# Optimization experiments

Hardware: AMD Instinct MI355X
Metric: run time of the kernel (lower is better)

## Reference

```python
import jax, jax.numpy as jnp
import numpy as np

B, S, E, H = 4, 2048, 1024, 16
D = E // H  # head_dim = 64

def setup_inputs() -> dict:
    key = jax.random.key(0)
    ks = jax.random.split(key, 9)
    std = 1.0 / np.sqrt(E)
    return {
        "x":  jax.random.normal(ks[0], (B, S, E), jnp.float32),
        "Wq": jax.random.uniform(ks[1], (E, E), jnp.float32, -std, std),
        "bq": jax.random.uniform(ks[2], (E,),   jnp.float32, -std, std),
        "Wk": jax.random.uniform(ks[3], (E, E), jnp.float32, -std, std),
        "bk": jax.random.uniform(ks[4], (E,),   jnp.float32, -std, std),
        "Wv": jax.random.uniform(ks[5], (E, E), jnp.float32, -std, std),
        "bv": jax.random.uniform(ks[6], (E,),   jnp.float32, -std, std),
        "Wo": jax.random.uniform(ks[7], (E, E), jnp.float32, -std, std),
        "bo": jax.random.uniform(ks[8], (E,),   jnp.float32, -std, std),
    }

def reference(x, Wq, bq, Wk, bk, Wv, bv, Wo, bo):
    b, s, e = x.shape
    # QKV projections (weights stored as [in,out] == torch W.T applied as x @ W)
    q = (x @ Wq + bq).reshape(b, s, H, D).transpose(0, 2, 1, 3)  # [B,H,S,D]
    k = (x @ Wk + bk).reshape(b, s, H, D).transpose(0, 2, 1, 3)
    v = (x @ Wv + bv).reshape(b, s, H, D).transpose(0, 2, 1, 3)
    scores = jnp.einsum('bhqd,bhkd->bhqk', q, k) / jnp.sqrt(jnp.float32(D))
    causal = jnp.triu(jnp.ones((s, s), bool), k=1)  # True above diagonal
    scores = jnp.where(causal, -jnp.inf, scores)
    p = jax.nn.softmax(scores, axis=-1)  # dropout disabled (eval mode)
    out = jnp.einsum('bhqk,bhkd->bhqd', p, v)  # [B,H,S,D]
    out = out.transpose(0, 2, 1, 3).reshape(b, s, e)
    return out @ Wo + bo
```

## Files before the change

kernel.cpp:

```cpp
#include <hip/hip_runtime.h>
#include <math.h>

#define E_DIM 1024
#define B_DIM 4
#define S_DIM 2048
#define H_DIM 16
#define D_HEAD 64
#define M_DIM (B_DIM * S_DIM)
#define LOG2E 1.44269504f

typedef _Float16 half8 __attribute__((ext_vector_type(8)));
typedef _Float16 half4 __attribute__((ext_vector_type(4)));
typedef __fp16  fp16x2 __attribute__((ext_vector_type(2)));
typedef float floatx4 __attribute__((ext_vector_type(4)));
typedef unsigned uint2v __attribute__((ext_vector_type(2)));
#define MFMA_F16(a, b, c) __builtin_amdgcn_mfma_f32_16x16x32_f16(a, b, c, 0, 0, 0)

#if __has_builtin(__builtin_amdgcn_exp2f)
#define EXP2F(x) __builtin_amdgcn_exp2f(x)
#else
#define EXP2F(x) exp2f(x)
#endif

union H4 { fp16x2 h2[2]; half4 h4; };
union H8 { fp16x2 h2[4]; half8 h8; };

#define GLDS16(g, l)                                                          \
    __builtin_amdgcn_global_load_lds(                                         \
        (const __attribute__((address_space(1))) void*)(g),                   \
        (__attribute__((address_space(3))) void*)(l), 16, 0, 0)

__device__ const int SEG_QBLK[40] = {3,4,5,6,7,7,8,8,9,9,10,10,11,11,11,12,12,12,
                                     13,13,13,14,14,14,15,15,15,15,
                                     2,6,10,14, 1,5,9,13, 0,4,8,12};
__device__ const int SEG_SEG[40]  = {0,0,0,0,0,1,0,1,0,1,0,1,0,1,2,0,1,2,
                                     0,1,2,0,1,2,0,1,2,3,
                                     0,1,2,3, 0,1,2,3, 0,1,2,3};
__device__ const int SEG_BASE[16] = {0,1,2,3,4,6,8,10,12,15,18,21,24,28,32,36};

__global__ __launch_bounds__(256) void cvt_x(
    const float* __restrict__ X, _Float16* __restrict__ Xh)
{
    size_t i = ((size_t)blockIdx.x * 256 + threadIdx.x) * 8;
    float4 a = *(const float4*)&X[i];
    float4 b = *(const float4*)&X[i + 4];
    half8 h = {(_Float16)a.x, (_Float16)a.y, (_Float16)a.z, (_Float16)a.w,
               (_Float16)b.x, (_Float16)b.y, (_Float16)b.z, (_Float16)b.w};
    *(half8*)&Xh[i] = h;
}

__global__ __launch_bounds__(256) void cvt_w(
    const float* __restrict__ W0, const float* __restrict__ W1,
    const float* __restrict__ W2, const float* __restrict__ W3,
    _Float16* __restrict__ T0, _Float16* __restrict__ T1,
    _Float16* __restrict__ T2, _Float16* __restrict__ T3)
{
    const int z = blockIdx.z;
    const float* W = (z == 0) ? W0 : (z == 1) ? W1 : (z == 2) ? W2 : W3;
    _Float16*   T  = (z == 0) ? T0 : (z == 1) ? T1 : (z == 2) ? T2 : T3;
    const int k0 = blockIdx.x * 64, n0 = blockIdx.y * 64;
    const int tid = threadIdx.x;
    __shared__ float t[64][65];
#pragma unroll
    for (int it = 0; it < 4; it++) {
        int r = it * 16 + (tid >> 4);
        int c = (tid & 15) * 4;
        float4 v = *(const float4*)&W[(size_t)(k0 + r) * E_DIM + n0 + c];
        t[r][c] = v.x; t[r][c + 1] = v.y; t[r][c + 2] = v.z; t[r][c + 3] = v.w;
    }
    __syncthreads();
#pragma unroll
    for (int it = 0; it < 2; it++) {
        int n = it * 32 + (tid >> 3);
        int kk = (tid & 7) * 8;
        half8 h;
#pragma unroll
        for (int j = 0; j < 8; j++) h[j] = (_Float16)t[kk + j][n];
        *(half8*)&T[(size_t)(n0 + n) * E_DIM + k0 + kk] = h;
    }
}

#define GEMM_CORE(Aptr, Bptr)                                                 \
    const int tid = threadIdx.x;                                              \
    const int wave = tid >> 6, lane = tid & 63;                               \
    const int m16 = lane & 15, quad = lane >> 4;                              \
    const int wm = (wave >> 1) * 64, wn = (wave & 1) * 64;                    \
    const int m0 = blockIdx.x * 128, n0 = blockIdx.y * 128;                   \
    __shared__ _Float16 As[128 * 32];                                         \
    __shared__ _Float16 Bs[128 * 32];                                         \
    floatx4 acc[4][4];                                                        \
    const floatx4 zf = {0.f, 0.f, 0.f, 0.f};                                  \
    _Pragma("unroll") for (int i = 0; i < 4; i++)                             \
        _Pragma("unroll") for (int j = 0; j < 4; j++) acc[i][j] = zf;         \
    const int lrow = lane >> 2, lseg = lane & 3;                              \
    const _Float16* gA = (Aptr) + (size_t)(m0 + wave * 32 + lrow) * E_DIM + lseg * 8; \
    const _Float16* gB = (Bptr) + (size_t)(n0 + wave * 32 + lrow) * E_DIM + lseg * 8; \
    _Float16* lA = As + (wave * 32) * 32;                                     \
    _Float16* lB = Bs + (wave * 32) * 32;                                     \
    for (int k0 = 0; k0 < E_DIM; k0 += 32) {                                  \
        __syncthreads();                                                      \
        GLDS16(gA + k0, lA);                                                  \
        GLDS16(gA + 16 * E_DIM + k0, lA + 16 * 32);                           \
        GLDS16(gB + k0, lB);                                                  \
        GLDS16(gB + 16 * E_DIM + k0, lB + 16 * 32);                           \
        __syncthreads();                                                      \
        half8 af[4], bf[4];                                                   \
        _Pragma("unroll") for (int mt = 0; mt < 4; mt++)                      \
            af[mt] = *(const half8*)&As[(wm + mt * 16 + m16) * 32 + quad * 8];\
        _Pragma("unroll") for (int nt = 0; nt < 4; nt++)                      \
            bf[nt] = *(const half8*)&Bs[(wn + nt * 16 + m16) * 32 + quad * 8];\
        _Pragma("unroll") for (int mt = 0; mt < 4; mt++)                      \
            _Pragma("unroll") for (int nt = 0; nt < 4; nt++)                  \
                acc[mt][nt] = MFMA_F16(af[mt], bf[nt], acc[mt][nt]);          \
    }

#define STAGE256(t, s)                                                        \
    _Pragma("unroll") for (int i = 0; i < 4; i++) {                           \
        GLDS16(aS[i] + (t) * 64, As + (s) * 16384 + dOff[i]);                 \
        GLDS16(bS[i] + (t) * 64, Bs + (s) * 16384 + dOff[i]);                 \
    }

#define PH_READ_A(mh)                                                         \
    _Pragma("unroll") for (int am = 0; am < 4; am++)                          \
        _Pragma("unroll") for (int kh = 0; kh < 2; kh++)                      \
            a_[am][kh] = *(const half8*)&As[sb +                              \
                (wr * 128 + (mh) * 64 + am * 16 + m16) * 64 +                 \
                (((kh * 4 + quad) ^ sw8) * 8)];

#define PH_READ_B(nh)                                                         \
    _Pragma("unroll") for (int bn = 0; bn < 2; bn++)                          \
        _Pragma("unroll") for (int kh = 0; kh < 2; kh++)                      \
            b_[bn][kh] = *(const half8*)&Bs[sb +                              \
                (wc * 64 + (nh) * 32 + bn * 16 + m16) * 64 +                  \
                (((kh * 4 + quad) ^ sw8) * 8)];

#define PH_MFMA(mh, nh)                                                       \
    __builtin_amdgcn_s_setprio(1);                                            \
    _Pragma("unroll") for (int am = 0; am < 4; am++)                          \
        _Pragma("unroll") for (int bn = 0; bn < 2; bn++)                      \
            acc[(mh) * 4 + am][(nh) * 2 + bn] =                               \
                MFMA_F16(a_[am][1], b_[bn][1],                                \
                    MFMA_F16(a_[am][0], b_[bn][0],                            \
                             acc[(mh) * 4 + am][(nh) * 2 + bn]));             \
    __builtin_amdgcn_s_setprio(0);

#define GEMM256_CORE(Aptr, Bptr)                                              \
    const int tid = threadIdx.x;                                              \
    const int wave = tid >> 6, lane = tid & 63;                               \
    const int m16 = lane & 15, quad = lane >> 4;                              \
    const int wr = wave >> 2, wc = wave & 3;                                  \
    const int m0 = blockIdx.x * 256, n0 = blockIdx.y * 256;                   \
    const int sw8 = m16 & 7;                                                  \
    __shared__ _Float16 As[2 * 16384];                                        \
    __shared__ _Float16 Bs[2 * 16384];                                        \
    floatx4 acc[8][4];                                                        \
    const floatx4 zf = {0.f, 0.f, 0.f, 0.f};                                  \
    _Pragma("unroll") for (int i = 0; i < 8; i++)                             \
        _Pragma("unroll") for (int j = 0; j < 4; j++) acc[i][j] = zf;         \
    const _Float16* aS[4];                                                    \
    const _Float16* bS[4];                                                    \
    int dOff[4];                                                              \
    _Pragma("unroll") for (int i = 0; i < 4; i++) {                           \
        int u = i * 512 + tid;                                                \
        int ru = u >> 3, cblk = (u & 7) ^ (ru & 7);                           \
        aS[i] = (Aptr) + (size_t)(m0 + ru) * E_DIM + cblk * 8;                \
        bS[i] = (Bptr) + (size_t)(n0 + ru) * E_DIM + cblk * 8;                \
        dOff[i] = i * 4096 + wave * 512;                                      \
    }                                                                         \
    STAGE256(0, 0);                                                           \
    STAGE256(1, 1);                                                           \
    asm volatile("s_waitcnt vmcnt(8)" ::: "memory");                          \
    __builtin_amdgcn_s_barrier();                                             \
    half8 a_[4][2], b_[2][2];                                                 \
    for (int t = 0; t < 16; t++) {                                            \
        const int sb = (t & 1) * 16384;                                       \
        PH_READ_A(0); PH_READ_B(0); PH_MFMA(0, 0);                            \
        PH_READ_B(1); PH_MFMA(0, 1);                                          \
        PH_READ_A(1); PH_MFMA(1, 1);                                          \
        PH_READ_B(0); PH_MFMA(1, 0);                                          \
        if (t + 1 < 16) {                                                     \
            asm volatile("s_waitcnt lgkmcnt(0)" ::: "memory");                \
            __builtin_amdgcn_s_barrier();                                     \
            if (t + 2 < 16) {                                                 \
                STAGE256(t + 2, t & 1);                                       \
                asm volatile("s_waitcnt vmcnt(8)" ::: "memory");              \
            } else {                                                          \
                asm volatile("s_waitcnt vmcnt(0)" ::: "memory");              \
            }                                                                 \
            __builtin_amdgcn_s_barrier();                                     \
        }                                                                     \
    }

__global__ __launch_bounds__(512) void qkv_mfma(
    const _Float16* __restrict__ Xh,
    const _Float16* __restrict__ Tq, const float* __restrict__ bq,
    const _Float16* __restrict__ Tk, const float* __restrict__ bk,
    const _Float16* __restrict__ Tv, const float* __restrict__ bv,
    _Float16* __restrict__ Qo, _Float16* __restrict__ Ko, _Float16* __restrict__ Vo)
{
    const int z = blockIdx.z;
    const _Float16* Wt   = (z == 0) ? Tq : (z == 1) ? Tk : Tv;
    const float*    bias = (z == 0) ? bq : (z == 1) ? bk : bv;

    GEMM256_CORE(Xh, Wt)

    if (z == 2) {
#pragma unroll
        for (int nt = 0; nt < 4; nt++) {
            int n = n0 + wc * 64 + nt * 16 + m16;
            int h = n >> 6, d = n & 63;
            int dt = d >> 4, ld = d & 15;
            float bias_v = bias[n];
#pragma unroll
            for (int mt = 0; mt < 8; mt++) {
                int m_b = m0 + wr * 128 + mt * 16 + quad * 4;
                int b = m_b >> 11, s = m_b & 2047;
                int bh = b * H_DIM + h;
                int c = s >> 6, kl = s & 63;
                int kh = kl >> 5, q8 = (kl >> 2) & 3, j0 = ((kl >> 4) & 1) * 4;
                size_t off = ((size_t)bh * 32 + c) * 4096
                           + (size_t)(((dt * 2 + kh) * 64 + q8 * 16 + ld) * 8 + j0);
                half4 hv;
#pragma unroll
                for (int r = 0; r < 4; r++) hv[r] = (_Float16)(acc[mt][nt][r] + bias_v);
                *(half4*)&Vo[off] = hv;
            }
        }
    } else {
        _Float16* Out = (z == 0) ? Qo : Ko;
        const float sc = (z == 0) ? 0.125f * LOG2E : 1.0f;
#pragma unroll
        for (int nt = 0; nt < 4; nt++) {
            int n = n0 + wc * 64 + nt * 16 + m16;
            int h = n >> 6, d = n & 63;
            int dh = d >> 5, qd = (d >> 3) & 3, j = d & 7;
            float bias_v = bias[n];
#pragma unroll
            for (int mt = 0; mt < 8; mt++) {
#pragma unroll
                for (int r = 0; r < 4; r++) {
                    int m = m0 + wr * 128 + mt * 16 + quad * 4 + r;
                    int b = m >> 11, s = m & 2047;
                    int bh = b * H_DIM + h;
                    size_t off;
                    if (z == 0) {
                        int qblk = s >> 7, qq = s & 127;
                        int sub = qq >> 4, lq = qq & 15;
                        off = ((size_t)bh * 16 + qblk) * 8192
                            + (size_t)(((sub * 2 + dh) * 64 + qd * 16 + lq) * 8 + j);
                    } else {
                        int c = s >> 6, kl = s & 63;
                        int kt = kl >> 4, lk = kl & 15;
                        off = ((size_t)bh * 32 + c) * 4096
                            + (size_t)(((kt * 2 + dh) * 64 + qd * 16 + lk) * 8 + j);
                    }
                    Out[off] = (_Float16)((acc[mt][nt][r] + bias_v) * sc);
                }
            }
        }
    }
}

__global__ __launch_bounds__(256) void out_mfma(
    const _Float16* __restrict__ Oh, const _Float16* __restrict__ To,
    const float* __restrict__ bias, float* __restrict__ Out)
{
    GEMM_CORE(Oh, To)

#pragma unroll
    for (int nt = 0; nt < 4; nt++) {
        int n = n0 + wn + nt * 16 + m16;
        float bias_v = bias[n];
#pragma unroll
        for (int mt = 0; mt < 4; mt++) {
#pragma unroll
            for (int r = 0; r < 4; r++) {
                int m = m0 + wm + mt * 16 + quad * 4 + r;
                Out[(size_t)m * E_DIM + n] = acc[mt][nt][r] + bias_v;
            }
        }
    }
}

__global__ __launch_bounds__(64) void attn_mfma(
    const _Float16* __restrict__ Qb, const _Float16* __restrict__ Kb,
    const _Float16* __restrict__ Vb, _Float16* __restrict__ Opart,
    float* __restrict__ Mv, float* __restrict__ Lv, _Float16* __restrict__ O)
{
    const int L = blockIdx.x;
    const int xcd = L & 7;
    const int u = L >> 3;
    const int bh = xcd * 8 + (u / 160);
    const int su = u % 160;
    const int wid = su >> 2;
    const int wave = su & 3;
    const int qblk = SEG_QBLK[wid];
    const int seg  = SEG_SEG[wid];
    const int q0 = qblk * 128;
    const int c0 = seg * 8;
    const int c1 = min(c0 + 8, 2 * qblk + 2);
    const bool solo = (c0 == 0) && (c1 == 2 * qblk + 2);
    const int lane = threadIdx.x;
    const int m16 = lane & 15, quad = lane >> 4;

    const int qmin = q0 + wave * 32;
    const int qmax = qmin + 31;
    const int c1w = min(c1, (qmax >> 6) + 1);

    const _Float16* gQ = Qb + ((size_t)bh * 16 + qblk) * 8192 + wave * 2048 + lane * 8;
    half8 qf[2][2];
#pragma unroll
    for (int mt = 0; mt < 2; mt++)
#pragma unroll
        for (int dh = 0; dh < 2; dh++)
            qf[mt][dh] = *(const half8*)&gQ[(mt * 2 + dh) * 512];

    const floatx4 zf  = {0.f, 0.f, 0.f, 0.f};
    const floatx4 cm4 = {-4.f, -4.f, -4.f, -4.f};
    half8 onev;
#pragma unroll
    for (int j = 0; j < 8; j++) onev[j] = (_Float16)1.0f;

    floatx4 acco[2][4];
    floatx4 lacc[2];
#pragma unroll
    for (int mt = 0; mt < 2; mt++) {
        lacc[mt] = zf;
#pragma unroll
        for (int dt = 0; dt < 4; dt++) acco[mt][dt] = zf;
    }

    const _Float16* gK = Kb + ((size_t)bh * 32 + c0) * 4096 + lane * 8;
    const _Float16* gV = Vb + ((size_t)bh * 32 + c0) * 4096 + lane * 8;

    half8 kf[4][2];
#pragma unroll
    for (int kt = 0; kt < 4; kt++)
#pragma unroll
        for (int dh = 0; dh < 2; dh++)
            kf[kt][dh] = *(const half8*)&gK[(kt * 2 + dh) * 512];
    gK += 4096;

    for (int c = c0; c < c1w; c++) {
        const int k0 = c * 64;

        half8 vf[4][2];
#pragma unroll
        for (int dt = 0; dt < 4; dt++)
#pragma unroll
            for (int kh = 0; kh < 2; kh++)
                vf[dt][kh] = *(const half8*)&gV[(dt * 2 + kh) * 512];
        gV += 4096;

        floatx4 sf[2][4];
        __builtin_amdgcn_s_setprio(1);
#pragma unroll
        for (int kt = 0; kt < 4; kt++)
#pragma unroll
            for (int mt = 0; mt < 2; mt++)
                sf[mt][kt] = MFMA_F16(kf[kt][1], qf[mt][1],
                               MFMA_F16(kf[kt][0], qf[mt][0], cm4));
        __builtin_amdgcn_s_setprio(0);

        if (c + 1 < c1w) {
#pragma unroll
            for (int kt = 0; kt < 4; kt++)
#pragma unroll
                for (int dh = 0; dh < 2; dh++)
                    kf[kt][dh] = *(const half8*)&gK[(kt * 2 + dh) * 512];
            gK += 4096;
        }

        const bool full = (k0 + 63 <= qmin);
#pragma unroll
        for (int mt = 0; mt < 2; mt++) {
            const int qg = qmin + mt * 16 + m16;
#pragma unroll
            for (int kt = 0; kt < 4; kt++)
#pragma unroll
                for (int r = 0; r < 4; r++) {
                    if (!full) {
                        int key = k0 + kt * 16 + quad * 4 + r;
                        if (key > qg) sf[mt][kt][r] = -INFINITY;
                    }
                }

            H8 u8[2];
#pragma unroll
            for (int kt = 0; kt < 4; kt++) {
                float e0 = EXP2F(sf[mt][kt][0]);
                float e1 = EXP2F(sf[mt][kt][1]);
                float e2 = EXP2F(sf[mt][kt][2]);
                float e3 = EXP2F(sf[mt][kt][3]);
                u8[kt >> 1].h2[(kt & 1) * 2]     = __builtin_amdgcn_cvt_pkrtz(e0, e1);
                u8[kt >> 1].h2[(kt & 1) * 2 + 1] = __builtin_amdgcn_cvt_pkrtz(e2, e3);
            }

            __builtin_amdgcn_s_setprio(1);
            lacc[mt] = MFMA_F16(onev, u8[1].h8,
                         MFMA_F16(onev, u8[0].h8, lacc[mt]));
#pragma unroll
            for (int dt = 0; dt < 4; dt++)
                acco[mt][dt] = MFMA_F16(vf[dt][1], u8[1].h8,
                                 MFMA_F16(vf[dt][0], u8[0].h8, acco[mt][dt]));
            __builtin_amdgcn_s_setprio(0);
        }
    }

    if (solo) {
        const int b = bh >> 4;
        const int h = bh & (H_DIM - 1);
#pragma unroll
        for (int mt = 0; mt < 2; mt++) {
            float inv = 1.f / lacc[mt][0];
            int q = qmin + mt * 16 + m16;
            _Float16* dst = O + (size_t)(b * S_DIM + q) * E_DIM + h * 64;
#pragma unroll
            for (int dt = 0; dt < 4; dt++) {
                H4 u4;
                u4.h2[0] = __builtin_amdgcn_cvt_pkrtz(acco[mt][dt][0] * inv, acco[mt][dt][1] * inv);
                u4.h2[1] = __builtin_amdgcn_cvt_pkrtz(acco[mt][dt][2] * inv, acco[mt][dt][3] * inv);
                *(half4*)&dst[dt * 16 + quad * 4] = u4.h4;
            }
        }
    } else {
        const size_t prow = ((size_t)bh * 40 + SEG_BASE[qblk] + seg) * 128;
#pragma unroll
        for (int mt = 0; mt < 2; mt++) {
            int lq = wave * 32 + mt * 16 + m16;
            if (quad == 0) {
                Lv[prow + lq] = lacc[mt][0];
            }
            _Float16* dst = Opart + (prow + lq) * 64;
#pragma unroll
            for (int dt = 0; dt < 4; dt++) {
                H4 u4;
                u4.h2[0] = __builtin_amdgcn_cvt_pkrtz(acco[mt][dt][0], acco[mt][dt][1]);
                u4.h2[1] = __builtin_amdgcn_cvt_pkrtz(acco[mt][dt][2], acco[mt][dt][3]);
                *(half4*)&dst[dt * 16 + quad * 4] = u4.h4;
            }
        }
    }
}

__global__ __launch_bounds__(256) void attn_combine(
    const _Float16* __restrict__ Opart, const float* __restrict__ Mv,
    const float* __restrict__ Lv, _Float16* __restrict__ O)
{
    const int qb = blockIdx.x + 4, bh = blockIdx.y;
    const int nseg = (qb >> 2) + 1;
    const size_t pbase = ((size_t)bh * 40 + SEG_BASE[qb]) * 128;
    const int t = threadIdx.x;
    const int r = t >> 1, dh = (t & 1) * 32;

    float L = 0.f;
    for (int s = 0; s < nseg; s++) L += Lv[pbase + s * 128 + r];
    const float invL = 1.f / L;

    const int b = bh >> 4, h = bh & (H_DIM - 1);
    const int q = qb * 128 + r;
    _Float16* dst = O + (size_t)(b * S_DIM + q) * E_DIM + h * 64 + dh;
#pragma unroll
    for (int d0 = 0; d0 < 32; d0 += 8) {
        float acc[8] = {0.f, 0.f, 0.f, 0.f, 0.f, 0.f, 0.f, 0.f};
        for (int s = 0; s < nseg; s++) {
            half8 v = *(const half8*)&Opart[(pbase + s * 128 + r) * 64 + dh + d0];
#pragma unroll
            for (int j = 0; j < 8; j++) acc[j] += (float)v[j];
        }
        half8 o;
#pragma unroll
        for (int j = 0; j < 8; j++) o[j] = (_Float16)(acc[j] * invL);
        *(half8*)&dst[d0] = o;
    }
}

extern "C" void kernel_launch(void* const* d_in, const int* in_sizes, int n_in,
                              void* d_out, int out_size, void* d_ws, size_t ws_size,
                              hipStream_t stream) {
    const float* x  = (const float*)d_in[0];
    const float* Wq = (const float*)d_in[1];
    const float* bq = (const float*)d_in[2];
    const float* Wk = (const float*)d_in[3];
    const float* bk = (const float*)d_in[4];
    const float* Wv = (const float*)d_in[5];
    const float* bv = (const float*)d_in[6];
    const float* Wo = (const float*)d_in[7];
    const float* bo = (const float*)d_in[8];

    const size_t SZ = (size_t)M_DIM * E_DIM;
    const size_t WZ = (size_t)E_DIM * E_DIM;
    _Float16* Xh = (_Float16*)d_ws;
    _Float16* Tq = Xh + SZ;
    _Float16* Tk = Tq + WZ;
    _Float16* Tv = Tk + WZ;
    _Float16* To = Tv + WZ;
    _Float16* Qb = To + WZ;
    _Float16* Kb = Qb + SZ;
    _Float16* Vb = Kb + SZ;
    _Float16* Opart = Vb + SZ;
    float* Mv = (float*)(Opart + (size_t)2560 * 8192);
    float* Lv = Mv + 2560 * 128;
    _Float16* Oh = Xh;

    cvt_x<<<dim3(M_DIM * E_DIM / 2048), 256, 0, stream>>>(x, Xh);
    cvt_w<<<dim3(16, 16, 4), 256, 0, stream>>>(Wq, Wk, Wv, Wo, Tq, Tk, Tv, To);

    qkv_mfma<<<dim3(M_DIM / 256, E_DIM / 256, 3), 512, 0, stream>>>(
        Xh, Tq, bq, Tk, bk, Tv, bv, Qb, Kb, Vb);

    attn_mfma<<<dim3(8 * 8 * 160), 64, 0, stream>>>(
        Qb, Kb, Vb, Opart, Mv, Lv, Oh);

    attn_combine<<<dim3(12, B_DIM * H_DIM), 256, 0, stream>>>(Opart, Mv, Lv, Oh);

    out_mfma<<<dim3(M_DIM / 128, E_DIM / 128), 256, 0, stream>>>(
        Oh, To, bo, (float*)d_out);
}
```

Baseline: 287.9 us.

## Use 128x128 double-buffered swizzled GEMM core for QKV and output projections

Replaces both the 256x256 QKV GEMM core and the simple single-buffered 128x128 output GEMM with one shared 128x128 core. The new core uses a 64-wide K step, XOR-swizzled LDS, double buffering and phased MFMA scheduling. The QKV kernel now launches 256-thread blocks over a 4x larger grid. The output projection gains load/compute overlap, while QKV trades per-block data reuse for more blocks and better occupancy.

New measurement: 280.7 us. -2.5%, faster.

```diff
diff --git a/kernel.cpp b/kernel.cpp
--- a/kernel.cpp
+++ b/kernel.cpp
@@ -80,109 +80,75 @@
     }
 }
 
-#define GEMM_CORE(Aptr, Bptr)                                                 \
+#define STAGE128(t, s)                                                        \
+    _Pragma("unroll") for (int i = 0; i < 4; i++) {                           \
+        GLDS16(aS[i] + (t) * 64, As + (s) * 8192 + dOff[i]);                  \
+        GLDS16(bS[i] + (t) * 64, Bs + (s) * 8192 + dOff[i]);                  \
+    }
+
+#define PH128_READ_A(mh)                                                      \
+    _Pragma("unroll") for (int am = 0; am < 2; am++)                          \
+        _Pragma("unroll") for (int kh = 0; kh < 2; kh++)                      \
+            a_[am][kh] = *(const half8*)&As[sb +                              \
+                (wr * 64 + ((mh) * 2 + am) * 16 + m16) * 64 +                 \
+                (((kh * 4 + quad) ^ sw8) * 8)];
+
+#define PH128_READ_B(nh)                                                      \
+    _Pragma("unroll") for (int bn = 0; bn < 2; bn++)                          \
+        _Pragma("unroll") for (int kh = 0; kh < 2; kh++)                      \
+            b_[bn][kh] = *(const half8*)&Bs[sb +                              \
+                (wc * 64 + ((nh) * 2 + bn) * 16 + m16) * 64 +                 \
+                (((kh * 4 + quad) ^ sw8) * 8)];
+
+#define PH128_MFMA(mh, nh)                                                    \
+    __builtin_amdgcn_s_setprio(1);                                            \
+    _Pragma("unroll") for (int am = 0; am < 2; am++)                          \
+        _Pragma("unroll") for (int bn = 0; bn < 2; bn++)                      \
+            acc[(mh) * 2 + am][(nh) * 2 + bn] =                               \
+                MFMA_F16(a_[am][1], b_[bn][1],                                \
+                    MFMA_F16(a_[am][0], b_[bn][0],                            \
+                             acc[(mh) * 2 + am][(nh) * 2 + bn]));             \
+    __builtin_amdgcn_s_setprio(0);
+
+#define GEMM128_CORE(Aptr, Bptr)                                              \
     const int tid = threadIdx.x;                                              \
     const int wave = tid >> 6, lane = tid & 63;                               \
     const int m16 = lane & 15, quad = lane >> 4;                              \
-    const int wm = (wave >> 1) * 64, wn = (wave & 1) * 64;                    \
+    const int wr = wave >> 1, wc = wave & 1;                                  \
     const int m0 = blockIdx.x * 128, n0 = blockIdx.y * 128;                   \
-    __shared__ _Float16 As[128 * 32];                                         \
-    __shared__ _Float16 Bs[128 * 32];                                         \
+    const int sw8 = m16 & 7;                                                  \
+    __shared__ _Float16 As[2 * 8192];                                         \
+    __shared__ _Float16 Bs[2 * 8192];                                         \
     floatx4 acc[4][4];                                                        \
     const floatx4 zf = {0.f, 0.f, 0.f, 0.f};                                  \
     _Pragma("unroll") for (int i = 0; i < 4; i++)                             \
-        _Pragma("unroll") for (int j = 0; j < 4; j++) acc[i][j] = zf;         \
-    const int lrow = lane >> 2, lseg = lane & 3;                              \
-    const _Float16* gA = (Aptr) + (size_t)(m0 + wave * 32 + lrow) * E_DIM + lseg * 8; \
-    const _Float16* gB = (Bptr) + (size_t)(n0 + wave * 32 + lrow) * E_DIM + lseg * 8; \
-    _Float16* lA = As + (wave * 32) * 32;                                     \
-    _Float16* lB = Bs + (wave * 32) * 32;                                     \
-    for (int k0 = 0; k0 < E_DIM; k0 += 32) {                                  \
-        __syncthreads();                                                      \
-        GLDS16(gA + k0, lA);                                                  \
-        GLDS16(gA + 16 * E_DIM + k0, lA + 16 * 32);                           \
-        GLDS16(gB + k0, lB);                                                  \
-        GLDS16(gB + 16 * E_DIM + k0, lB + 16 * 32);                           \
-        __syncthreads();                                                      \
-        half8 af[4], bf[4];                                                   \
-        _Pragma("unroll") for (int mt = 0; mt < 4; mt++)                      \
-            af[mt] = *(const half8*)&As[(wm + mt * 16 + m16) * 32 + quad * 8];\
-        _Pragma("unroll") for (int nt = 0; nt < 4; nt++)                      \
-            bf[nt] = *(const half8*)&Bs[(wn + nt * 16 + m16) * 32 + quad * 8];\
-        _Pragma("unroll") for (int mt = 0; mt < 4; mt++)                      \
-            _Pragma("unroll") for (int nt = 0; nt < 4; nt++)                  \
-                acc[mt][nt] = MFMA_F16(af[mt], bf[nt], acc[mt][nt]);          \
-    }
-
-#define STAGE256(t, s)                                                        \
-    _Pragma("unroll") for (int i = 0; i < 4; i++) {                           \
-        GLDS16(aS[i] + (t) * 64, As + (s) * 16384 + dOff[i]);                 \
-        GLDS16(bS[i] + (t) * 64, Bs + (s) * 16384 + dOff[i]);                 \
-    }
-
-#define PH_READ_A(mh)                                                         \
-    _Pragma("unroll") for (int am = 0; am < 4; am++)                          \
-        _Pragma("unroll") for (int kh = 0; kh < 2; kh++)                      \
-            a_[am][kh] = *(const half8*)&As[sb +                              \
-                (wr * 128 + (mh) * 64 + am * 16 + m16) * 64 +                 \
-                (((kh * 4 + quad) ^ sw8) * 8)];
-
-#define PH_READ_B(nh)                                                         \
-    _Pragma("unroll") for (int bn = 0; bn < 2; bn++)                          \
-        _Pragma("unroll") for (int kh = 0; kh < 2; kh++)                      \
-            b_[bn][kh] = *(const half8*)&Bs[sb +                              \
-                (wc * 64 + (nh) * 32 + bn * 16 + m16) * 64 +                  \
-                (((kh * 4 + quad) ^ sw8) * 8)];
-
-#define PH_MFMA(mh, nh)                                                       \
-    __builtin_amdgcn_s_setprio(1);                                            \
-    _Pragma("unroll") for (int am = 0; am < 4; am++)                          \
-        _Pragma("unroll") for (int bn = 0; bn < 2; bn++)                      \
-            acc[(mh) * 4 + am][(nh) * 2 + bn] =                               \
-                MFMA_F16(a_[am][1], b_[bn][1],                                \
-                    MFMA_F16(a_[am][0], b_[bn][0],                            \
-                             acc[(mh) * 4 + am][(nh) * 2 + bn]));             \
-    __builtin_amdgcn_s_setprio(0);
-
-#define GEMM256_CORE(Aptr, Bptr)                                              \
-    const int tid = threadIdx.x;                                              \
-    const int wave = tid >> 6, lane = tid & 63;                               \
-    const int m16 = lane & 15, quad = lane >> 4;                              \
-    const int wr = wave >> 2, wc = wave & 3;                                  \
-    const int m0 = blockIdx.x * 256, n0 = blockIdx.y * 256;                   \
-    const int sw8 = m16 & 7;                                                  \
-    __shared__ _Float16 As[2 * 16384];                                        \
-    __shared__ _Float16 Bs[2 * 16384];                                        \
-    floatx4 acc[8][4];                                                        \
-    const floatx4 zf = {0.f, 0.f, 0.f, 0.f};                                  \
-    _Pragma("unroll") for (int i = 0; i < 8; i++)                             \
         _Pragma("unroll") for (int j = 0; j < 4; j++) acc[i][j] = zf;         \
     const _Float16* aS[4];                                                    \
     const _Float16* bS[4];                                                    \
     int dOff[4];                                                              \
     _Pragma("unroll") for (int i = 0; i < 4; i++) {                           \
-        int u = i * 512 + tid;                                                \
-        int ru = u >> 3, cblk = (u & 7) ^ (ru & 7);                           \
-        aS[i] = (Aptr) + (size_t)(m0 + ru) * E_DIM + cblk * 8;                \
-        bS[i] = (Bptr) + (size_t)(n0 + ru) * E_DIM + cblk * 8;                \
-        dOff[i] = i * 4096 + wave * 512;                                      \
+        int u = i * 256 + tid;                                                \
+        int ru = u >> 3, cb = (u & 7) ^ (ru & 7);                             \
+        aS[i] = (Aptr) + (size_t)(m0 + ru) * E_DIM + cb * 8;                  \
+        bS[i] = (Bptr) + (size_t)(n0 + ru) * E_DIM + cb * 8;                  \
+        dOff[i] = i * 2048 + wave * 512;                                      \
     }                                                                         \
-    STAGE256(0, 0);                                                           \
-    STAGE256(1, 1);                                                           \
+    STAGE128(0, 0);                                                           \
+    STAGE128(1, 1);                                                           \
     asm volatile("s_waitcnt vmcnt(8)" ::: "memory");                          \
     __builtin_amdgcn_s_barrier();                                             \
-    half8 a_[4][2], b_[2][2];                                                 \
+    half8 a_[2][2], b_[2][2];                                                 \
     for (int t = 0; t < 16; t++) {                                            \
-        const int sb = (t & 1) * 16384;                                       \
-        PH_READ_A(0); PH_READ_B(0); PH_MFMA(0, 0);                            \
-        PH_READ_B(1); PH_MFMA(0, 1);                                          \
-        PH_READ_A(1); PH_MFMA(1, 1);                                          \
-        PH_READ_B(0); PH_MFMA(1, 0);                                          \
+        const int sb = (t & 1) * 8192;                                        \
+        PH128_READ_A(0); PH128_READ_B(0); PH128_MFMA(0, 0);                   \
+        PH128_READ_B(1); PH128_MFMA(0, 1);                                    \
+        PH128_READ_A(1); PH128_MFMA(1, 1);                                    \
+        PH128_READ_B(0); PH128_MFMA(1, 0);                                    \
         if (t + 1 < 16) {                                                     \
             asm volatile("s_waitcnt lgkmcnt(0)" ::: "memory");                \
             __builtin_amdgcn_s_barrier();                                     \
             if (t + 2 < 16) {                                                 \
-                STAGE256(t + 2, t & 1);                                       \
+                STAGE128(t + 2, t & 1);                                       \
                 asm volatile("s_waitcnt vmcnt(8)" ::: "memory");              \
             } else {                                                          \
                 asm volatile("s_waitcnt vmcnt(0)" ::: "memory");              \
@@ -191,7 +157,7 @@
         }                                                                     \
     }
 
-__global__ __launch_bounds__(512) void qkv_mfma(
+__global__ __launch_bounds__(256) void qkv_mfma(
     const _Float16* __restrict__ Xh,
     const _Float16* __restrict__ Tq, const float* __restrict__ bq,
     const _Float16* __restrict__ Tk, const float* __restrict__ bk,
@@ -202,7 +168,7 @@
     const _Float16* Wt   = (z == 0) ? Tq : (z == 1) ? Tk : Tv;
     const float*    bias = (z == 0) ? bq : (z == 1) ? bk : bv;
 
-    GEMM256_CORE(Xh, Wt)
+    GEMM128_CORE(Xh, Wt)
 
     if (z == 2) {
 #pragma unroll
@@ -212,8 +178,8 @@
             int dt = d >> 4, ld = d & 15;
             float bias_v = bias[n];
 #pragma unroll
-            for (int mt = 0; mt < 8; mt++) {
-                int m_b = m0 + wr * 128 + mt * 16 + quad * 4;
+            for (int mt = 0; mt < 4; mt++) {
+                int m_b = m0 + wr * 64 + mt * 16 + quad * 4;
                 int b = m_b >> 11, s = m_b & 2047;
                 int bh = b * H_DIM + h;
                 int c = s >> 6, kl = s & 63;
@@ -236,10 +202,10 @@
             int dh = d >> 5, qd = (d >> 3) & 3, j = d & 7;
             float bias_v = bias[n];
 #pragma unroll
-            for (int mt = 0; mt < 8; mt++) {
+            for (int mt = 0; mt < 4; mt++) {
 #pragma unroll
                 for (int r = 0; r < 4; r++) {
-                    int m = m0 + wr * 128 + mt * 16 + quad * 4 + r;
+                    int m = m0 + wr * 64 + mt * 16 + quad * 4 + r;
                     int b = m >> 11, s = m & 2047;
                     int bh = b * H_DIM + h;
                     size_t off;
@@ -265,17 +231,17 @@
     const _Float16* __restrict__ Oh, const _Float16* __restrict__ To,
     const float* __restrict__ bias, float* __restrict__ Out)
 {
-    GEMM_CORE(Oh, To)
+    GEMM128_CORE(Oh, To)
 
 #pragma unroll
     for (int nt = 0; nt < 4; nt++) {
-        int n = n0 + wn + nt * 16 + m16;
+        int n = n0 + wc * 64 + nt * 16 + m16;
         float bias_v = bias[n];
 #pragma unroll
         for (int mt = 0; mt < 4; mt++) {
 #pragma unroll
             for (int r = 0; r < 4; r++) {
-                int m = m0 + wm + mt * 16 + quad * 4 + r;
+                int m = m0 + wr * 64 + mt * 16 + quad * 4 + r;
                 Out[(size_t)m * E_DIM + n] = acc[mt][nt][r] + bias_v;
             }
         }
@@ -506,7 +472,7 @@
     cvt_x<<<dim3(M_DIM * E_DIM / 2048), 256, 0, stream>>>(x, Xh);
     cvt_w<<<dim3(16, 16, 4), 256, 0, stream>>>(Wq, Wk, Wv, Wo, Tq, Tk, Tv, To);
 
-    qkv_mfma<<<dim3(M_DIM / 256, E_DIM / 256, 3), 512, 0, stream>>>(
+    qkv_mfma<<<dim3(M_DIM / 128, E_DIM / 128, 3), 256, 0, stream>>>(
         Xh, Tq, bq, Tk, bk, Tv, bv, Qb, Kb, Vb);
 
     attn_mfma<<<dim3(8 * 8 * 160), 64, 0, stream>>>(
```
